# Performance work log

Measured on AMD Instinct MI355X. Metric: run time of the kernel, lower is better.

Reference implementation:

```python
import jax, jax.numpy as jnp
import numpy as np

N = 8192
TD, ID, D = 768, 1024, 1024
E = 8
GH = D // 2  # gate hidden
EPS = 1e-5


def _init_linear(key, fan_in, shape):
    # torch nn.Linear default init: U(-1/sqrt(fan_in), 1/sqrt(fan_in))
    bound = 1.0 / np.sqrt(fan_in)
    return jax.random.uniform(key, shape, jnp.float32, -bound, bound)


def setup_inputs() -> dict:
    key = jax.random.key(0)
    ks = jax.random.split(key, 16)
    return {
        "text_features": jax.random.normal(ks[0], (N, TD), jnp.float32),
        "image_features": jax.random.normal(ks[1], (N, ID), jnp.float32),
        "Wt": _init_linear(ks[2], TD, (TD, D)),
        "bt": _init_linear(ks[3], TD, (D,)),
        "Wi": _init_linear(ks[4], ID, (ID, D)),
        "bi": _init_linear(ks[5], ID, (D,)),
        "eW1": _init_linear(ks[6], 2 * D, (E, 2 * D, D)),
        "eb1": _init_linear(ks[7], 2 * D, (E, D)),
        "eW2": _init_linear(ks[8], D, (E, D, D)),
        "eb2": _init_linear(ks[9], D, (E, D)),
        "ln_g": jnp.ones((E, D), jnp.float32),
        "ln_b": jnp.zeros((E, D), jnp.float32),
        "gW1": _init_linear(ks[10], 2 * D, (2 * D, GH)),
        "gb1": _init_linear(ks[11], 2 * D, (GH,)),
        "gW2": _init_linear(ks[12], GH, (GH, E)),
        "gb2": _init_linear(ks[13], GH, (E,)),
    }


def reference(text_features, image_features, Wt, bt, Wi, bi,
              eW1, eb1, eW2, eb2, ln_g, ln_b, gW1, gb1, gW2, gb2):
    # project both modalities to shared dim D (dropout is identity in eval)
    ta = text_features @ Wt + bt            # [N, D]
    ia = image_features @ Wi + bi           # [N, D]
    c = jnp.concatenate([ta, ia], axis=-1)  # [N, 2D]

    # gating MLP -> softmax over experts
    gh = jax.nn.silu(c @ gW1 + gb1)                      # [N, GH]
    w = jax.nn.softmax(gh @ gW2 + gb2, axis=-1)          # [N, E]

    # all experts densely, batched over E
    h = jax.nn.silu(jnp.einsum('nc,ecd->ned', c, eW1) + eb1)   # [N, E, D]
    o = jnp.einsum('ned,edf->nef', h, eW2) + eb2               # [N, E, D]

    # per-expert LayerNorm over last dim
    mu = o.mean(axis=-1, keepdims=True)
    var = ((o - mu) ** 2).mean(axis=-1, keepdims=True)
    o = (o - mu) * jax.lax.rsqrt(var + EPS) * ln_g + ln_b      # [N, E, D]

    # gate-weighted sum over experts
    return jnp.einsum('ned,ne->nd', o, w)                      # [N, D]
```

## Files before the change

kernel.cpp:

```cpp
#include <hip/hip_runtime.h>

#define NROWS 8192
#define TDIM 768
#define IDIM 1024
#define DDIM 1024
#define NEXP 8
#define GHID 512

typedef __attribute__((ext_vector_type(8))) short short8;
typedef __attribute__((ext_vector_type(4))) float f4;
typedef __attribute__((ext_vector_type(4))) unsigned short us4;

__device__ __forceinline__ unsigned short f2bf(float f) {
  union { float f; unsigned u; } v; v.f = f;
  unsigned r = v.u + 0x7FFF + ((v.u >> 16) & 1);
  return (unsigned short)(r >> 16);
}
__device__ __forceinline__ float bf2f(unsigned short u) {
  union { unsigned u; float f; } v; v.u = ((unsigned)u) << 16;
  return v.f;
}

__device__ __forceinline__ void gload16(const void* g, void* l) {
  __builtin_amdgcn_global_load_lds(
      (const __attribute__((address_space(1))) void*)g,
      (__attribute__((address_space(3))) void*)l, 16, 0, 0);
}

__global__ __launch_bounds__(256) void cast_bf16_kernel(
    const float* __restrict__ src, unsigned short* __restrict__ dst, int n4) {
  int i = blockIdx.x * 256 + threadIdx.x;
  if (i < n4) {
    f4 v = ((const f4*)src)[i];
    us4 o;
    o[0] = f2bf(v[0]); o[1] = f2bf(v[1]); o[2] = f2bf(v[2]); o[3] = f2bf(v[3]);
    ((us4*)dst)[i] = o;
  }
}

__global__ __launch_bounds__(256) void transpose_cast_kernel(
    const float* __restrict__ src, unsigned short* __restrict__ dst, int R, int C) {
  __shared__ float tile[32][33];
  size_t base = (size_t)blockIdx.z * R * C;
  int c0 = blockIdx.x * 32, r0 = blockIdx.y * 32;
  int tx = threadIdx.x, ty = threadIdx.y;
#pragma unroll
  for (int j = 0; j < 32; j += 8)
    tile[ty + j][tx] = src[base + (size_t)(r0 + ty + j) * C + c0 + tx];
  __syncthreads();
#pragma unroll
  for (int j = 0; j < 32; j += 8)
    dst[base + (size_t)(c0 + ty + j) * R + r0 + tx] = f2bf(tile[tx][ty + j]);
}

template <int SILU, int OUTBF>
__global__ __launch_bounds__(512, 1) void gemm256_kernel(
    const unsigned short* __restrict__ A, const unsigned short* __restrict__ BT,
    const float* __restrict__ bias, void* __restrict__ Cptr,
    int K, int lda, int ldb, int ldc,
    size_t sA, size_t sB, size_t sBias, size_t sC) {
  __shared__ __align__(16) char LDS[131072];

  const unsigned short* Ab = A + (size_t)blockIdx.z * sA;
  const unsigned short* Bb = BT + (size_t)blockIdx.z * sB;
  const float* biasb = bias + (size_t)blockIdx.z * sBias;

  const int gx = gridDim.x;
  const int nwg = gx * gridDim.y;
  const int orig = blockIdx.y * gx + blockIdx.x;
  const int q = nwg >> 3, r = nwg & 7;
  const int xcd = orig & 7, idx = orig >> 3;
  const int wgid = (xcd < r ? xcd * (q + 1) : r * (q + 1) + (xcd - r) * q) + idx;
  const int bx = wgid % gx, by = wgid / gx;

  const int tid = threadIdx.x;
  const int wave = tid >> 6, lane = tid & 63;
  const int wm = wave >> 2, wn = wave & 3;
  const int row0 = by * 256, col0 = bx * 256;

  f4 acc[8][4] = {};

  const int srow = tid >> 3;
  const int scolg = ((tid & 7) << 4) ^ (((tid >> 3) & 7) << 4);
  const size_t lda2 = (size_t)lda * 2, ldb2 = (size_t)ldb * 2;
  const char* Abytes = (const char*)Ab;
  const char* Bbytes = (const char*)Bb;
  const size_t aG = (size_t)(row0 + srow) * lda2 + scolg;
  const size_t bG = (size_t)(col0 + srow) * ldb2 + scolg;
  char* ldsw = LDS + wave * 1024;

  const int aBase = (wm * 128 + (lane & 15)) * 128;
  const int bBase = 32768 + (wn * 64 + (lane & 15)) * 128;
  const int ck0 = ((lane >> 4) << 4) ^ ((lane & 7) << 4);

  const int NT = K >> 6;

#pragma unroll
  for (int p = 0; p < 4; p++)
    gload16(Abytes + aG + (size_t)(p * 64) * lda2, ldsw + p * 8192);
#pragma unroll
  for (int p = 0; p < 4; p++)
    gload16(Bbytes + bG + (size_t)(p * 64) * ldb2, ldsw + 32768 + p * 8192);

  for (int t = 0; t < NT; t++) {
    const int buf = (t & 1) << 16;
    const int nbuf = 65536 - buf;
    __builtin_amdgcn_s_barrier();
    __builtin_amdgcn_sched_barrier(0);
    if (t + 1 < NT) {
      const size_t kb = (size_t)(t + 1) << 7;
#pragma unroll
      for (int p = 0; p < 4; p++)
        gload16(Abytes + aG + (size_t)(p * 64) * lda2 + kb, ldsw + nbuf + p * 8192);
#pragma unroll
      for (int p = 0; p < 4; p++)
        gload16(Bbytes + bG + (size_t)(p * 64) * ldb2 + kb, ldsw + nbuf + 32768 + p * 8192);
      asm volatile("s_waitcnt vmcnt(8)" ::: "memory");
    } else {
      asm volatile("s_waitcnt vmcnt(0)" ::: "memory");
    }
    __builtin_amdgcn_s_barrier();
    __builtin_amdgcn_sched_barrier(0);
#pragma unroll
    for (int kk = 0; kk < 2; kk++) {
      const int ck = ck0 ^ (kk << 6);
      short8 av[8], bv[4];
#pragma unroll
      for (int m = 0; m < 8; m++)
        av[m] = *(const short8*)(LDS + buf + aBase + m * 2048 + ck);
#pragma unroll
      for (int n = 0; n < 4; n++)
        bv[n] = *(const short8*)(LDS + buf + bBase + n * 2048 + ck);
#pragma unroll
      for (int m = 0; m < 8; m++)
#pragma unroll
        for (int n = 0; n < 4; n++)
          acc[m][n] = __builtin_amdgcn_mfma_f32_16x16x32_bf16(av[m], bv[n], acc[m][n], 0, 0, 0);
    }
  }

  const int crow0 = row0 + wm * 128 + (lane >> 4) * 4;
  const int ccol0 = col0 + wn * 64 + (lane & 15);
  char* Cb = (char*)Cptr + (size_t)blockIdx.z * sC * (OUTBF ? 2 : 4);
#pragma unroll
  for (int n = 0; n < 4; n++) {
    const int col = ccol0 + n * 16;
    const float bvv = biasb[col];
#pragma unroll
    for (int m = 0; m < 8; m++) {
#pragma unroll
      for (int r2 = 0; r2 < 4; r2++) {
        float v = acc[m][n][r2] + bvv;
        if (SILU) v = v / (1.0f + __expf(-v));
        const size_t cidx = (size_t)(crow0 + m * 16 + r2) * ldc + col;
        if (OUTBF) ((unsigned short*)Cb)[cidx] = f2bf(v);
        else       ((float*)Cb)[cidx] = v;
      }
    }
  }
}

template <int SILU, int OUTBF>
__global__ __launch_bounds__(256) void gemm_tn_kernel(
    const unsigned short* __restrict__ A, const unsigned short* __restrict__ BT,
    const float* __restrict__ bias, void* __restrict__ Cptr,
    int K, int lda, int ldb, int ldc,
    size_t sA, size_t sB, size_t sBias, size_t sC) {
  __shared__ unsigned short Als[128 * 32];
  __shared__ unsigned short Bls[128 * 32];

  const unsigned short* Ab = A + (size_t)blockIdx.z * sA;
  const unsigned short* Bb = BT + (size_t)blockIdx.z * sB;
  const float* biasb = bias + (size_t)blockIdx.z * sBias;

  const int gx = gridDim.x;
  const int nwg = gx * gridDim.y;
  const int orig = blockIdx.y * gx + blockIdx.x;
  const int q = nwg >> 3, r = nwg & 7;
  const int xcd = orig & 7, idx = orig >> 3;
  const int wgid = (xcd < r ? xcd * (q + 1) : r * (q + 1) + (xcd - r) * q) + idx;
  const int bx = wgid % gx, by = wgid / gx;

  const int tid = threadIdx.x;
  const int wave = tid >> 6, lane = tid & 63;
  const int row0 = by * 128, col0 = bx * 128;
  const int wm = wave >> 1, wn = wave & 1;
  f4 acc[4][4] = {};

  const int aoff = (wm * 64 + (lane & 15)) * 32 + (lane >> 4) * 8;
  const int boff = (wn * 64 + (lane & 15)) * 32 + (lane >> 4) * 8;

  const int L0 = tid, L1 = tid + 256;
  const size_t aofs0 = (size_t)(row0 + (L0 >> 2)) * lda + (L0 & 3) * 8;
  const size_t aofs1 = (size_t)(row0 + (L1 >> 2)) * lda + (L1 & 3) * 8;
  const size_t bofs0 = (size_t)(col0 + (L0 >> 2)) * ldb + (L0 & 3) * 8;
  const size_t bofs1 = (size_t)(col0 + (L1 >> 2)) * ldb + (L1 & 3) * 8;
  char* abase0 = (char*)Als + wave * 1024;
  char* abase1 = (char*)Als + 4096 + wave * 1024;
  char* bbase0 = (char*)Bls + wave * 1024;
  char* bbase1 = (char*)Bls + 4096 + wave * 1024;

  for (int k0 = 0; k0 < K; k0 += 32) {
    gload16(Ab + aofs0 + k0, abase0);
    gload16(Ab + aofs1 + k0, abase1);
    gload16(Bb + bofs0 + k0, bbase0);
    gload16(Bb + bofs1 + k0, bbase1);
    __syncthreads();
    short8 af[4], bfr[4];
#pragma unroll
    for (int i = 0; i < 4; i++) af[i] = *(const short8*)&Als[aoff + i * 512];
#pragma unroll
    for (int j = 0; j < 4; j++) bfr[j] = *(const short8*)&Bls[boff + j * 512];
#pragma unroll
    for (int i = 0; i < 4; i++)
#pragma unroll
      for (int j = 0; j < 4; j++)
        acc[i][j] = __builtin_amdgcn_mfma_f32_16x16x32_bf16(af[i], bfr[j], acc[i][j], 0, 0, 0);
    __syncthreads();
  }

  const int crow = row0 + wm * 64 + (lane >> 4) * 4;
  const int ccol = col0 + wn * 64 + (lane & 15);
  char* Cb = (char*)Cptr + (size_t)blockIdx.z * sC * (OUTBF ? 2 : 4);
#pragma unroll
  for (int j = 0; j < 4; j++) {
    const int col = ccol + j * 16;
    const float bv = biasb[col];
#pragma unroll
    for (int i = 0; i < 4; i++) {
#pragma unroll
      for (int r2 = 0; r2 < 4; r2++) {
        float v = acc[i][j][r2] + bv;
        if (SILU) v = v / (1.0f + __expf(-v));
        const size_t cidx = (size_t)(crow + i * 16 + r2) * ldc + col;
        if (OUTBF)
          ((unsigned short*)Cb)[cidx] = f2bf(v);
        else
          ((float*)Cb)[cidx] = v;
      }
    }
  }
}

__global__ __launch_bounds__(256) void gate_kernel(
    const unsigned short* __restrict__ gh, const float* __restrict__ gW2,
    const float* __restrict__ gb2, float* __restrict__ wout) {
  __shared__ float sW[NEXP * GHID];
  int tid = threadIdx.x;
  for (int i = tid; i < GHID * NEXP; i += 256) {
    int k = i >> 3, e = i & 7;
    sW[e * GHID + k] = gW2[i];
  }
  __syncthreads();
  int wave = tid >> 6, lane = tid & 63;
  int row = blockIdx.x * 4 + wave;
  float acc[NEXP] = {};
#pragma unroll
  for (int i = 0; i < 8; i++) {
    int k = lane + 64 * i;
    float x = bf2f(gh[(size_t)row * GHID + k]);
#pragma unroll
    for (int e = 0; e < NEXP; e++) acc[e] += x * sW[e * GHID + k];
  }
#pragma unroll
  for (int off = 32; off; off >>= 1)
#pragma unroll
    for (int e = 0; e < NEXP; e++) acc[e] += __shfl_xor(acc[e], off);
  float lg[NEXP], mx = -1e30f;
#pragma unroll
  for (int e = 0; e < NEXP; e++) { lg[e] = acc[e] + gb2[e]; mx = fmaxf(mx, lg[e]); }
  float s = 0.f;
#pragma unroll
  for (int e = 0; e < NEXP; e++) { lg[e] = __expf(lg[e] - mx); s += lg[e]; }
  if (lane < NEXP) wout[(size_t)row * NEXP + lane] = lg[lane] / s;
}

__global__ __launch_bounds__(256) void ln_acc8_kernel(
    const float* __restrict__ o, const float* __restrict__ wgate,
    const float* __restrict__ ln_g, const float* __restrict__ ln_b,
    float* __restrict__ out, int row0) {
  int wave = threadIdx.x >> 6, lane = threadIdx.x & 63;
  int lrow = blockIdx.x * 4 + wave;
  int grow = row0 + lrow;
  float res[16];
#pragma unroll
  for (int u = 0; u < 16; u++) res[u] = 0.f;
#pragma unroll
  for (int e = 0; e < NEXP; e++) {
    const float* orow = o + (size_t)lrow * (NEXP * DDIM) + (size_t)e * DDIM;
    float xs[16];
    float s = 0.f, s2 = 0.f;
#pragma unroll
    for (int qq = 0; qq < 4; qq++) {
      f4 t = *(const f4*)&orow[qq * 256 + lane * 4];
#pragma unroll
      for (int u = 0; u < 4; u++) {
        xs[qq * 4 + u] = t[u];
        s += t[u];
        s2 += t[u] * t[u];
      }
    }
#pragma unroll
    for (int off = 32; off; off >>= 1) {
      s += __shfl_xor(s, off);
      s2 += __shfl_xor(s2, off);
    }
    const float inv = 1.0f / 1024.0f;
    float mu = s * inv;
    float var = s2 * inv - mu * mu;
    float rr = rsqrtf(var + 1e-5f);
    float wv = wgate[(size_t)grow * NEXP + e];
#pragma unroll
    for (int qq = 0; qq < 4; qq++) {
      int d = qq * 256 + lane * 4;
      f4 gg = *(const f4*)&ln_g[(size_t)e * DDIM + d];
      f4 bb = *(const f4*)&ln_b[(size_t)e * DDIM + d];
#pragma unroll
      for (int u = 0; u < 4; u++)
        res[qq * 4 + u] += wv * ((xs[qq * 4 + u] - mu) * rr * gg[u] + bb[u]);
    }
  }
  size_t rowbase = (size_t)grow * DDIM;
#pragma unroll
  for (int qq = 0; qq < 4; qq++) {
    f4 t;
#pragma unroll
    for (int u = 0; u < 4; u++) t[u] = res[qq * 4 + u];
    *(f4*)&out[rowbase + qq * 256 + lane * 4] = t;
  }
}

extern "C" void kernel_launch(void* const* d_in, const int* in_sizes, int n_in,
                              void* d_out, int out_size, void* d_ws, size_t ws_size,
                              hipStream_t stream) {
  const float* text  = (const float*)d_in[0];
  const float* image = (const float*)d_in[1];
  const float* Wt    = (const float*)d_in[2];
  const float* bt    = (const float*)d_in[3];
  const float* Wi    = (const float*)d_in[4];
  const float* bi    = (const float*)d_in[5];
  const float* eW1   = (const float*)d_in[6];
  const float* eb1   = (const float*)d_in[7];
  const float* eW2   = (const float*)d_in[8];
  const float* eb2   = (const float*)d_in[9];
  const float* ln_g  = (const float*)d_in[10];
  const float* ln_b  = (const float*)d_in[11];
  const float* gW1   = (const float*)d_in[12];
  const float* gb1   = (const float*)d_in[13];
  const float* gW2   = (const float*)d_in[14];
  const float* gb2   = (const float*)d_in[15];
  float* out = (float*)d_out;

  size_t off = 0;
  auto alloc = [&](size_t bytes) -> void* {
    void* p = (char*)d_ws + off;
    off += (bytes + 255) & ~(size_t)255;
    return p;
  };
  unsigned short* eW1T = (unsigned short*)alloc((size_t)NEXP * 2 * DDIM * DDIM * 2);
  unsigned short* eW2T = (unsigned short*)alloc((size_t)NEXP * DDIM * DDIM * 2);
  unsigned short* c_bf = (unsigned short*)alloc((size_t)NROWS * 2 * DDIM * 2);
  float* wgate         = (float*)alloc((size_t)NROWS * NEXP * 4);
  const size_t overlay0 = off;

  unsigned short* text_bf = (unsigned short*)alloc((size_t)NROWS * TDIM * 2);
  unsigned short* img_bf  = (unsigned short*)alloc((size_t)NROWS * IDIM * 2);
  unsigned short* WtT     = (unsigned short*)alloc((size_t)TDIM * DDIM * 2);
  unsigned short* WiT     = (unsigned short*)alloc((size_t)IDIM * DDIM * 2);
  unsigned short* gW1T    = (unsigned short*)alloc((size_t)2 * DDIM * GHID * 2);
  unsigned short* gh_bf   = (unsigned short*)alloc((size_t)NROWS * GHID * 2);

  int slab = 8192;
  while (slab > 256 &&
         overlay0 + (size_t)slab * (size_t)(2 * NEXP * DDIM + 4 * NEXP * DDIM) > ws_size)
    slab >>= 1;
  unsigned short* h_slab = (unsigned short*)((char*)d_ws + overlay0);
  float* o_slab = (float*)((char*)d_ws + overlay0 + (size_t)slab * NEXP * DDIM * 2);

  cast_bf16_kernel<<<(NROWS * TDIM / 4 + 255) / 256, 256, 0, stream>>>(text, text_bf, NROWS * TDIM / 4);
  cast_bf16_kernel<<<(NROWS * IDIM / 4 + 255) / 256, 256, 0, stream>>>(image, img_bf, NROWS * IDIM / 4);

  transpose_cast_kernel<<<dim3(DDIM / 32, TDIM / 32, 1), dim3(32, 8), 0, stream>>>(Wt, WtT, TDIM, DDIM);
  transpose_cast_kernel<<<dim3(DDIM / 32, IDIM / 32, 1), dim3(32, 8), 0, stream>>>(Wi, WiT, IDIM, DDIM);
  transpose_cast_kernel<<<dim3(GHID / 32, 2 * DDIM / 32, 1), dim3(32, 8), 0, stream>>>(gW1, gW1T, 2 * DDIM, GHID);
  transpose_cast_kernel<<<dim3(DDIM / 32, 2 * DDIM / 32, NEXP), dim3(32, 8), 0, stream>>>(eW1, eW1T, 2 * DDIM, DDIM);
  transpose_cast_kernel<<<dim3(DDIM / 32, DDIM / 32, NEXP), dim3(32, 8), 0, stream>>>(eW2, eW2T, DDIM, DDIM);

  gemm_tn_kernel<0, 1><<<dim3(DDIM / 128, NROWS / 128), 256, 0, stream>>>(
      text_bf, WtT, bt, c_bf, TDIM, TDIM, TDIM, 2 * DDIM, 0, 0, 0, 0);
  gemm_tn_kernel<0, 1><<<dim3(DDIM / 128, NROWS / 128), 256, 0, stream>>>(
      img_bf, WiT, bi, c_bf + DDIM, IDIM, IDIM, IDIM, 2 * DDIM, 0, 0, 0, 0);

  gemm_tn_kernel<1, 1><<<dim3(GHID / 128, NROWS / 128), 256, 0, stream>>>(
      c_bf, gW1T, gb1, gh_bf, 2 * DDIM, 2 * DDIM, 2 * DDIM, GHID, 0, 0, 0, 0);

  gate_kernel<<<NROWS / 4, 256, 0, stream>>>(gh_bf, gW2, gb2, wgate);

  for (int r0 = 0; r0 < NROWS; r0 += slab) {
    gemm256_kernel<1, 1><<<dim3(NEXP * DDIM / 256, slab / 256), 512, 0, stream>>>(
        c_bf + (size_t)r0 * 2 * DDIM, eW1T, eb1, h_slab,
        2 * DDIM, 2 * DDIM, 2 * DDIM, NEXP * DDIM, 0, 0, 0, 0);
    gemm256_kernel<0, 0><<<dim3(DDIM / 256, slab / 256, NEXP), 512, 0, stream>>>(
        h_slab, eW2T, eb2, o_slab,
        DDIM, NEXP * DDIM, DDIM, NEXP * DDIM,
        (size_t)DDIM, (size_t)DDIM * DDIM, (size_t)DDIM, (size_t)DDIM);
    ln_acc8_kernel<<<slab / 4, 256, 0, stream>>>(o_slab, wgate, ln_g, ln_b, out, r0);
  }
}
```

Before: 743.9 us.

## Interleave next-tile global loads with MFMA phases in GEMM main loop

The GEMM K-loop now runs in four phases, each computing two M-subtiles. The next tile's global-to-LDS loads are spread across those phases instead of being issued all at once before compute, and s_setprio raises priority around the MFMA blocks. B fragments are loaded once per tile and reused across phases. This aims to overlap memory traffic with matrix math and lower register pressure, at the cost of extra barriers per tile.

```diff
diff --git a/kernel.cpp b/kernel.cpp
--- a/kernel.cpp
+++ b/kernel.cpp
@@ -102,40 +102,80 @@
   for (int p = 0; p < 4; p++)
     gload16(Bbytes + bG + (size_t)(p * 64) * ldb2, ldsw + 32768 + p * 8192);
 
+  short8 bv[4][2];
   for (int t = 0; t < NT; t++) {
     const int buf = (t & 1) << 16;
     const int nbuf = 65536 - buf;
+    const size_t kb = (size_t)(t + 1) << 7;
+    const bool more = (t + 1 < NT);
+
+    if (more) {
+      gload16(Abytes + aG + kb, ldsw + nbuf);
+      gload16(Abytes + aG + (size_t)64 * lda2 + kb, ldsw + nbuf + 8192);
+      asm volatile("s_waitcnt vmcnt(2)" ::: "memory");
+    } else {
+      asm volatile("s_waitcnt vmcnt(0)" ::: "memory");
+    }
     __builtin_amdgcn_s_barrier();
     __builtin_amdgcn_sched_barrier(0);
-    if (t + 1 < NT) {
-      const size_t kb = (size_t)(t + 1) << 7;
-#pragma unroll
-      for (int p = 0; p < 4; p++)
-        gload16(Abytes + aG + (size_t)(p * 64) * lda2 + kb, ldsw + nbuf + p * 8192);
-#pragma unroll
-      for (int p = 0; p < 4; p++)
-        gload16(Bbytes + bG + (size_t)(p * 64) * ldb2 + kb, ldsw + nbuf + 32768 + p * 8192);
-      asm volatile("s_waitcnt vmcnt(8)" ::: "memory");
-    } else {
-      asm volatile("s_waitcnt vmcnt(0)" ::: "memory");
+    {
+      short8 av[2][2];
+#pragma unroll
+      for (int n = 0; n < 4; n++)
+#pragma unroll
+        for (int kk = 0; kk < 2; kk++)
+          bv[n][kk] = *(const short8*)(LDS + buf + bBase + n * 2048 + (ck0 ^ (kk << 6)));
+#pragma unroll
+      for (int m = 0; m < 2; m++)
+#pragma unroll
+        for (int kk = 0; kk < 2; kk++)
+          av[m][kk] = *(const short8*)(LDS + buf + aBase + m * 2048 + (ck0 ^ (kk << 6)));
+      asm volatile("s_waitcnt lgkmcnt(0)" ::: "memory");
+      __builtin_amdgcn_sched_barrier(0);
+      __builtin_amdgcn_s_setprio(1);
+#pragma unroll
+      for (int kk = 0; kk < 2; kk++)
+#pragma unroll
+        for (int m = 0; m < 2; m++)
+#pragma unroll
+          for (int n = 0; n < 4; n++)
+            acc[m][n] = __builtin_amdgcn_mfma_f32_16x16x32_bf16(av[m][kk], bv[n][kk], acc[m][n], 0, 0, 0);
+      __builtin_amdgcn_s_setprio(0);
     }
     __builtin_amdgcn_s_barrier();
-    __builtin_amdgcn_sched_barrier(0);
-#pragma unroll
-    for (int kk = 0; kk < 2; kk++) {
-      const int ck = ck0 ^ (kk << 6);
-      short8 av[8], bv[4];
-#pragma unroll
-      for (int m = 0; m < 8; m++)
-        av[m] = *(const short8*)(LDS + buf + aBase + m * 2048 + ck);
-#pragma unroll
-      for (int n = 0; n < 4; n++)
-        bv[n] = *(const short8*)(LDS + buf + bBase + n * 2048 + ck);
-#pragma unroll
-      for (int m = 0; m < 8; m++)
-#pragma unroll
-        for (int n = 0; n < 4; n++)
-          acc[m][n] = __builtin_amdgcn_mfma_f32_16x16x32_bf16(av[m], bv[n], acc[m][n], 0, 0, 0);
+
+#pragma unroll
+    for (int ph = 1; ph < 4; ph++) {
+      if (more) {
+        if (ph == 1) {
+          gload16(Abytes + aG + (size_t)128 * lda2 + kb, ldsw + nbuf + 16384);
+          gload16(Abytes + aG + (size_t)192 * lda2 + kb, ldsw + nbuf + 24576);
+        } else if (ph == 2) {
+          gload16(Bbytes + bG + kb, ldsw + nbuf + 32768);
+          gload16(Bbytes + bG + (size_t)64 * ldb2 + kb, ldsw + nbuf + 40960);
+        } else {
+          gload16(Bbytes + bG + (size_t)128 * ldb2 + kb, ldsw + nbuf + 49152);
+          gload16(Bbytes + bG + (size_t)192 * ldb2 + kb, ldsw + nbuf + 57344);
+        }
+      }
+      short8 av[2][2];
+#pragma unroll
+      for (int m = 0; m < 2; m++)
+#pragma unroll
+        for (int kk = 0; kk < 2; kk++)
+          av[m][kk] = *(const short8*)(LDS + buf + aBase + (ph * 2 + m) * 2048 + (ck0 ^ (kk << 6)));
+      asm volatile("s_waitcnt lgkmcnt(0)" ::: "memory");
+      __builtin_amdgcn_sched_barrier(0);
+      __builtin_amdgcn_s_setprio(1);
+#pragma unroll
+      for (int kk = 0; kk < 2; kk++)
+#pragma unroll
+        for (int m = 0; m < 2; m++)
+#pragma unroll
+          for (int n = 0; n < 4; n++)
+            acc[ph * 2 + m][n] = __builtin_amdgcn_mfma_f32_16x16x32_bf16(av[m][kk], bv[n][kk], acc[ph * 2 + m][n], 0, 0, 0);
+      __builtin_amdgcn_s_setprio(0);
+      __builtin_amdgcn_s_barrier();
     }
   }
 
```

Result: faster. 719.3 us (-3.3%).
